# Performance work log

Hardware: AMD Instinct MI355X
Metric: run time of the kernel (lower is better)

The kernel has to match this reference:

```python
import jax, jax.numpy as jnp
import numpy as np

N, M, C_IN, C_OUT = 16384, 8192, 128, 64
P_EDGE = 0.005  # ~41 hyperedges per vertex


def setup_inputs() -> dict:
    key = jax.random.key(0)
    k1, k2, k3, k4 = jax.random.split(key, 4)
    X = jax.random.normal(k1, (N, C_IN), dtype=jnp.float32)
    # 0/1 incidence matrix (dense realization of a sparse hypergraph)
    H = (jax.random.uniform(k2, (N, M)) < P_EDGE).astype(jnp.float32)
    W = jax.random.normal(k3, (C_OUT, C_IN), dtype=jnp.float32) / np.sqrt(C_IN)
    b = jax.random.normal(k4, (C_OUT,), dtype=jnp.float32) * 0.01
    return {"X": X, "H": H, "W": W, "b": b}


def reference(X, H, W, b):
    # theta: linear projection  (N, C_in) -> (N, C_out)
    Xt = X @ W.T + b
    # D_v^{-1/2} and D_e^{-1} with torch-style nan_to_num semantics
    dv = jnp.nan_to_num(jnp.power(H.sum(axis=1), -0.5))  # (N,)
    de = jnp.nan_to_num(jnp.power(H.sum(axis=0), -1.0))  # (M,)
    # L @ X = diag(dv) H diag(de) H^T diag(dv) @ Xt, applied as row scalings
    # (W_e is the identity in the original code)
    Y = dv[:, None] * Xt           # (N, C_out)
    Y = H.T @ Y                    # (M, C_out) gather to hyperedges
    Y = de[:, None] * Y            # (M, C_out)
    Y = H @ Y                      # (N, C_out) scatter back to vertices
    Y = dv[:, None] * Y            # (N, C_out)
    # is_last=False -> ReLU; bn=None; dropout is identity in eval mode
    return jax.nn.relu(Y)
```

## Files before the change

kernel.cpp:

```cpp
#include <hip/hip_runtime.h>
#include <hip/hip_bf16.h>
#include <stdint.h>

#define N_V   16384
#define M_E   8192
#define CIN   128
#define COUT  64
#define RCAP  128
#define CCAP  192
#define BCAP  16
#define CHUNKS 64
#define RPC   (N_V / CHUNKS)

#define OFF_ROWCNT  0
#define OFF_COLCNT  (N_V * 4)
#define OFF_ROWLIST (OFF_COLCNT + M_E * 4)
#define OFF_COLLIST (OFF_ROWLIST + N_V * RCAP * 2)
#define OFF_YV      (OFF_COLLIST + M_E * CCAP * 2)
#define OFF_E       (OFF_YV + N_V * COUT * 4)
#define OFF_HIST    (OFF_E + M_E * COUT * 4)

__global__ __launch_bounds__(256) void k_rows(
    const uint4* __restrict__ H4,
    int* __restrict__ row_cnt, unsigned short* __restrict__ row_list) {
  __shared__ unsigned short bucket[4][BCAP + 1][64];
  int wid  = threadIdx.x >> 6;
  int lane = threadIdx.x & 63;
  int n    = blockIdx.x * 4 + wid;
  const uint4* rp = H4 + (size_t)n * (M_E / 4) + lane;
  unsigned short (*bk)[64] = bucket[wid];
  int cnt = 0;
  int mb  = lane * 4;
#pragma unroll 8
  for (int it = 0; it < (M_E / 4) / 64; ++it) {
    uint4 v = rp[it * 64];
    int w;
    w = cnt > BCAP ? BCAP : cnt; bk[w][lane] = (unsigned short)(mb + 0); cnt += (v.x != 0u);
    w = cnt > BCAP ? BCAP : cnt; bk[w][lane] = (unsigned short)(mb + 1); cnt += (v.y != 0u);
    w = cnt > BCAP ? BCAP : cnt; bk[w][lane] = (unsigned short)(mb + 2); cnt += (v.z != 0u);
    w = cnt > BCAP ? BCAP : cnt; bk[w][lane] = (unsigned short)(mb + 3); cnt += (v.w != 0u);
    mb += 256;
  }
  if (cnt > BCAP) cnt = BCAP;
  int pfx = cnt;
#pragma unroll
  for (int s = 1; s < 64; s <<= 1) {
    int t = __shfl_up(pfx, s, 64);
    if (lane >= s) pfx += t;
  }
  int total = __shfl(pfx, 63, 64);
  int start = pfx - cnt;
  unsigned short* rl = row_list + n * RCAP;
  for (int k = 0; k < cnt; ++k) {
    int p = start + k;
    if (p < RCAP) rl[p] = bk[k][lane];
  }
  if (lane == 63) row_cnt[n] = total > RCAP ? RCAP : total;
}

__global__ __launch_bounds__(256) void k_hist(
    const int* __restrict__ row_cnt, const unsigned short* __restrict__ row_list,
    unsigned int* __restrict__ hist) {
  __shared__ unsigned int h[M_E];
  for (int i = threadIdx.x; i < M_E; i += 256) h[i] = 0u;
  __syncthreads();
  int n = blockIdx.x * RPC + threadIdx.x;
  int cnt = row_cnt[n];
  const unsigned short* lst = row_list + n * RCAP;
  for (int i = 0; i < cnt; ++i) atomicAdd(&h[lst[i]], 1u);
  __syncthreads();
  unsigned int* out = hist + (size_t)blockIdx.x * M_E;
  for (int i = threadIdx.x; i < M_E; i += 256) out[i] = h[i];
}

__global__ __launch_bounds__(256) void k_scan(
    unsigned int* __restrict__ hist, int* __restrict__ col_cnt) {
  int e = blockIdx.x * 256 + threadIdx.x;
  unsigned int run = 0;
#pragma unroll 8
  for (int c = 0; c < CHUNKS; ++c) {
    unsigned int hv = hist[(size_t)c * M_E + e];
    hist[(size_t)c * M_E + e] = run;
    run += hv;
  }
  col_cnt[e] = (int)run;
}

__global__ __launch_bounds__(256) void k_fill(
    const int* __restrict__ row_cnt, const unsigned short* __restrict__ row_list,
    const unsigned int* __restrict__ hist, unsigned short* __restrict__ col_list) {
  __shared__ unsigned int h[M_E];
  const unsigned int* base = hist + (size_t)blockIdx.x * M_E;
  for (int i = threadIdx.x; i < M_E; i += 256) h[i] = base[i];
  __syncthreads();
  int n = blockIdx.x * RPC + threadIdx.x;
  int cnt = row_cnt[n];
  const unsigned short* lst = row_list + n * RCAP;
  for (int i = 0; i < cnt; ++i) {
    int e = lst[i];
    unsigned int slot = atomicAdd(&h[e], 1u);
    if (slot < CCAP) col_list[e * CCAP + slot] = (unsigned short)n;
  }
}

__global__ __launch_bounds__(256) void k_project(
    const float* __restrict__ X, const float* __restrict__ W,
    const float* __restrict__ b, const int* __restrict__ row_cnt,
    float* __restrict__ Yv) {
  int wid  = threadIdx.x >> 6;
  int lane = threadIdx.x & 63;
  int cb   = __builtin_amdgcn_readfirstlane(wid);
  int n    = blockIdx.x * 64 + lane;
  const float* xrow  = X + n * CIN;
  const float* wbase = W + cb * 16 * CIN;

  float acc[16];
#pragma unroll
  for (int j = 0; j < 16; ++j) acc[j] = 0.f;

  for (int k4 = 0; k4 < CIN / 4; ++k4) {
    float4 x = *(const float4*)(xrow + k4 * 4);
#pragma unroll
    for (int j = 0; j < 16; ++j) {
      float4 w = *(const float4*)(wbase + j * CIN + k4 * 4);
      acc[j] += x.x * w.x + x.y * w.y + x.z * w.z + x.w * w.w;
    }
  }

  int cnt  = row_cnt[n];
  float dv = cnt > 0 ? rsqrtf((float)cnt) : 0.f;
  float* yrow = Yv + n * COUT + cb * 16;
#pragma unroll
  for (int g = 0; g < 4; ++g) {
    float4 o;
    o.x = dv * (acc[4 * g + 0] + b[cb * 16 + 4 * g + 0]);
    o.y = dv * (acc[4 * g + 1] + b[cb * 16 + 4 * g + 1]);
    o.z = dv * (acc[4 * g + 2] + b[cb * 16 + 4 * g + 2]);
    o.w = dv * (acc[4 * g + 3] + b[cb * 16 + 4 * g + 3]);
    *(float4*)(yrow + 4 * g) = o;
  }
}

__global__ __launch_bounds__(256) void k_edge(
    const float* __restrict__ Yv, const int* __restrict__ col_cnt,
    const unsigned short* __restrict__ col_list, float* __restrict__ E) {
  int wid  = threadIdx.x >> 6;
  int lane = threadIdx.x & 63;
  int m    = blockIdx.x * 4 + wid;
  int realcnt = col_cnt[m];
  int cnt  = realcnt > CCAP ? CCAP : realcnt;
  const unsigned short* lst = col_list + m * CCAP;
  float acc = 0.f;
  int i = 0;
  for (; i + 8 <= cnt; i += 8) {
    uint4 u = *(const uint4*)(lst + i);
    int n0 = u.x & 0xffff, n1 = u.x >> 16;
    int n2 = u.y & 0xffff, n3 = u.y >> 16;
    int n4 = u.z & 0xffff, n5 = u.z >> 16;
    int n6 = u.w & 0xffff, n7 = u.w >> 16;
    float a0 = Yv[n0 * COUT + lane];
    float a1 = Yv[n1 * COUT + lane];
    float a2 = Yv[n2 * COUT + lane];
    float a3 = Yv[n3 * COUT + lane];
    float a4 = Yv[n4 * COUT + lane];
    float a5 = Yv[n5 * COUT + lane];
    float a6 = Yv[n6 * COUT + lane];
    float a7 = Yv[n7 * COUT + lane];
    acc += ((a0 + a1) + (a2 + a3)) + ((a4 + a5) + (a6 + a7));
  }
  for (; i < cnt; ++i) acc += Yv[(int)lst[i] * COUT + lane];
  float den = realcnt > 0 ? 1.f / (float)realcnt : 0.f;
  E[m * COUT + lane] = den * acc;
}

__global__ __launch_bounds__(256) void k_vertex(
    const float* __restrict__ E, const int* __restrict__ row_cnt,
    const unsigned short* __restrict__ row_list, float* __restrict__ out) {
  int wid  = threadIdx.x >> 6;
  int lane = threadIdx.x & 63;
  int n    = blockIdx.x * 4 + wid;
  int cnt  = row_cnt[n];
  const unsigned short* lst = row_list + n * RCAP;
  float acc = 0.f;
  int i = 0;
  for (; i + 8 <= cnt; i += 8) {
    uint4 u = *(const uint4*)(lst + i);
    int m0 = u.x & 0xffff, m1 = u.x >> 16;
    int m2 = u.y & 0xffff, m3 = u.y >> 16;
    int m4 = u.z & 0xffff, m5 = u.z >> 16;
    int m6 = u.w & 0xffff, m7 = u.w >> 16;
    float a0 = E[m0 * COUT + lane];
    float a1 = E[m1 * COUT + lane];
    float a2 = E[m2 * COUT + lane];
    float a3 = E[m3 * COUT + lane];
    float a4 = E[m4 * COUT + lane];
    float a5 = E[m5 * COUT + lane];
    float a6 = E[m6 * COUT + lane];
    float a7 = E[m7 * COUT + lane];
    acc += ((a0 + a1) + (a2 + a3)) + ((a4 + a5) + (a6 + a7));
  }
  for (; i < cnt; ++i) acc += E[(int)lst[i] * COUT + lane];
  float dv = cnt > 0 ? rsqrtf((float)cnt) : 0.f;
  out[n * COUT + lane] = fmaxf(dv * acc, 0.f);
}

extern "C" void kernel_launch(void* const* d_in, const int* in_sizes, int n_in,
                              void* d_out, int out_size, void* d_ws, size_t ws_size,
                              hipStream_t stream) {
  const float* X = (const float*)d_in[0];
  const float* H = (const float*)d_in[1];
  const float* W = (const float*)d_in[2];
  const float* b = (const float*)d_in[3];
  float* out = (float*)d_out;

  char* ws = (char*)d_ws;
  int* row_cnt = (int*)(ws + OFF_ROWCNT);
  int* col_cnt = (int*)(ws + OFF_COLCNT);
  unsigned short* row_list = (unsigned short*)(ws + OFF_ROWLIST);
  unsigned short* col_list = (unsigned short*)(ws + OFF_COLLIST);
  float* Yv = (float*)(ws + OFF_YV);
  float* E  = (float*)(ws + OFF_E);
  unsigned int* hist = (unsigned int*)(ws + OFF_HIST);

  k_rows<<<N_V / 4, 256, 0, stream>>>((const uint4*)H, row_cnt, row_list);
  k_hist<<<CHUNKS, 256, 0, stream>>>(row_cnt, row_list, hist);
  k_scan<<<M_E / 256, 256, 0, stream>>>(hist, col_cnt);
  k_fill<<<CHUNKS, 256, 0, stream>>>(row_cnt, row_list, hist, col_list);
  k_project<<<N_V / 64, 256, 0, stream>>>(X, W, b, row_cnt, Yv);
  k_edge<<<M_E / 4, 256, 0, stream>>>(Yv, col_cnt, col_list, E);
  k_vertex<<<N_V / 4, 256, 0, stream>>>(E, row_cnt, row_list, out);
}
```

Before: 753.5 us.

## Build column lists with global atomics inside row extraction kernel

Fuses the CSR-to-CSC transpose into the row-scanning kernel. Each found nonzero atomically claims a slot in its hyperedge's column list, which removes the separate histogram, scan and fill kernels and their low-parallelism 64-block launches. This adds global atomic contention on column counters, and the column order becomes nondeterministic, which changes the floating-point summation order.

Measured after the change: 734.6 us. 2.5% less time.

```diff
diff --git a/kernel.cpp b/kernel.cpp
--- a/kernel.cpp
+++ b/kernel.cpp
@@ -9,8 +9,6 @@
 #define RCAP  128
 #define CCAP  192
 #define BCAP  16
-#define CHUNKS 64
-#define RPC   (N_V / CHUNKS)
 
 #define OFF_ROWCNT  0
 #define OFF_COLCNT  (N_V * 4)
@@ -18,11 +16,11 @@
 #define OFF_COLLIST (OFF_ROWLIST + N_V * RCAP * 2)
 #define OFF_YV      (OFF_COLLIST + M_E * CCAP * 2)
 #define OFF_E       (OFF_YV + N_V * COUT * 4)
-#define OFF_HIST    (OFF_E + M_E * COUT * 4)
 
 __global__ __launch_bounds__(256) void k_rows(
     const uint4* __restrict__ H4,
-    int* __restrict__ row_cnt, unsigned short* __restrict__ row_list) {
+    int* __restrict__ row_cnt, unsigned short* __restrict__ row_list,
+    int* __restrict__ col_cnt, unsigned short* __restrict__ col_list) {
   __shared__ unsigned short bucket[4][BCAP + 1][64];
   int wid  = threadIdx.x >> 6;
   int lane = threadIdx.x & 63;
@@ -53,54 +51,12 @@
   unsigned short* rl = row_list + n * RCAP;
   for (int k = 0; k < cnt; ++k) {
     int p = start + k;
-    if (p < RCAP) rl[p] = bk[k][lane];
+    int e = bk[k][lane];
+    if (p < RCAP) rl[p] = (unsigned short)e;
+    int cp = atomicAdd(&col_cnt[e], 1);
+    if (cp < CCAP) col_list[e * CCAP + cp] = (unsigned short)n;
   }
   if (lane == 63) row_cnt[n] = total > RCAP ? RCAP : total;
-}
-
-__global__ __launch_bounds__(256) void k_hist(
-    const int* __restrict__ row_cnt, const unsigned short* __restrict__ row_list,
-    unsigned int* __restrict__ hist) {
-  __shared__ unsigned int h[M_E];
-  for (int i = threadIdx.x; i < M_E; i += 256) h[i] = 0u;
-  __syncthreads();
-  int n = blockIdx.x * RPC + threadIdx.x;
-  int cnt = row_cnt[n];
-  const unsigned short* lst = row_list + n * RCAP;
-  for (int i = 0; i < cnt; ++i) atomicAdd(&h[lst[i]], 1u);
-  __syncthreads();
-  unsigned int* out = hist + (size_t)blockIdx.x * M_E;
-  for (int i = threadIdx.x; i < M_E; i += 256) out[i] = h[i];
-}
-
-__global__ __launch_bounds__(256) void k_scan(
-    unsigned int* __restrict__ hist, int* __restrict__ col_cnt) {
-  int e = blockIdx.x * 256 + threadIdx.x;
-  unsigned int run = 0;
-#pragma unroll 8
-  for (int c = 0; c < CHUNKS; ++c) {
-    unsigned int hv = hist[(size_t)c * M_E + e];
-    hist[(size_t)c * M_E + e] = run;
-    run += hv;
-  }
-  col_cnt[e] = (int)run;
-}
-
-__global__ __launch_bounds__(256) void k_fill(
-    const int* __restrict__ row_cnt, const unsigned short* __restrict__ row_list,
-    const unsigned int* __restrict__ hist, unsigned short* __restrict__ col_list) {
-  __shared__ unsigned int h[M_E];
-  const unsigned int* base = hist + (size_t)blockIdx.x * M_E;
-  for (int i = threadIdx.x; i < M_E; i += 256) h[i] = base[i];
-  __syncthreads();
-  int n = blockIdx.x * RPC + threadIdx.x;
-  int cnt = row_cnt[n];
-  const unsigned short* lst = row_list + n * RCAP;
-  for (int i = 0; i < cnt; ++i) {
-    int e = lst[i];
-    unsigned int slot = atomicAdd(&h[e], 1u);
-    if (slot < CCAP) col_list[e * CCAP + slot] = (unsigned short)n;
-  }
 }
 
 __global__ __launch_bounds__(256) void k_project(
@@ -220,12 +176,11 @@
   unsigned short* col_list = (unsigned short*)(ws + OFF_COLLIST);
   float* Yv = (float*)(ws + OFF_YV);
   float* E  = (float*)(ws + OFF_E);
-  unsigned int* hist = (unsigned int*)(ws + OFF_HIST);
 
-  k_rows<<<N_V / 4, 256, 0, stream>>>((const uint4*)H, row_cnt, row_list);
-  k_hist<<<CHUNKS, 256, 0, stream>>>(row_cnt, row_list, hist);
-  k_scan<<<M_E / 256, 256, 0, stream>>>(hist, col_cnt);
-  k_fill<<<CHUNKS, 256, 0, stream>>>(row_cnt, row_list, hist, col_list);
+  hipMemsetAsync(col_cnt, 0, M_E * 4, stream);
+
+  k_rows<<<N_V / 4, 256, 0, stream>>>((const uint4*)H, row_cnt, row_list,
+                                      col_cnt, col_list);
   k_project<<<N_V / 64, 256, 0, stream>>>(X, W, b, row_cnt, Yv);
   k_edge<<<M_E / 4, 256, 0, stream>>>(Yv, col_cnt, col_list, E);
   k_vertex<<<N_V / 4, 256, 0, stream>>>(E, row_cnt, row_list, out);
```
